# Optimization experiments

Hardware: AMD Instinct MI355X
Metric: run time of the kernel (lower is better)

Reference implementation:

```python
import jax, jax.numpy as jnp
import numpy as np

N_STEPS = 4  # fixed-step RK4 stand-in for dopri5 (jit-friendly, same ODE math)

def mlp(params, tt, z):
    # tt: [N,1] time, z: [N,dim] -> velocity [N,dim]
    W1, b1, W2, b2, W3, b3 = params
    h = jnp.tanh(jnp.concatenate([z, tt], axis=-1) @ W1 + b1)
    h = jnp.tanh(h @ W2 + b2)
    return h @ W3 + b3

def f_and_div(params, tt, z):
    # brute-force divergence via dim JVPs (dim=3, exact trace)
    f = lambda zz: mlp(params, tt, zz)
    out = f(z)
    div = jnp.zeros((z.shape[0],), z.dtype)
    for i in range(z.shape[1]):
        tang = jnp.zeros_like(z).at[:, i].set(1.0)
        _, jv = jax.jvp(f, (z,), (tang,))
        div = div + jv[:, i]
    return out, div[:, None]

def dyn(params, s, t0, z):
    # reparametrize per-sample integration t: t0 -> 0 onto s in [0,1]; dt/ds = -t0
    tt = t0 * (1.0 - s)
    f, div = f_and_div(params, tt, z)
    dz = -t0 * f                                   # dz/ds
    ddiv = t0 * div                                # accumulates int_0^{t0} div f dt
    dpen = t0 * jnp.sum(f * f, axis=-1, keepdims=True)  # kinetic-energy OT penalty
    return dz, ddiv, dpen

def integrate_to_t0(params, x, t0):
    h = 1.0 / N_STEPS
    z = x
    d = jnp.zeros((x.shape[0], 1), x.dtype)
    p = jnp.zeros_like(d)
    for k in range(N_STEPS):
        s = k * h
        g = lambda s_, z_: dyn(params, s_, t0, z_)
        k1z, k1d, k1p = g(s, z)
        k2z, k2d, k2p = g(s + 0.5 * h, z + 0.5 * h * k1z)
        k3z, k3d, k3p = g(s + 0.5 * h, z + 0.5 * h * k2z)
        k4z, k4d, k4p = g(s + h, z + h * k3z)
        z = z + (h / 6.0) * (k1z + 2 * k2z + 2 * k3z + k4z)
        d = d + (h / 6.0) * (k1d + 2 * k2d + 2 * k3d + k4d)
        p = p + (h / 6.0) * (k1p + 2 * k2p + 2 * k3p + k4p)
    return z, d, p

def grid_sample_3d_zeros(vol, coords):
    # vol: [D,H,W]; coords: [N,3] in (x,y,z) normalized [-1,1], align_corners=False,
    # padding_mode='zeros' (matches torch grid_sample semantics)
    D, H, W = vol.shape
    px = ((coords[:, 0] + 1.0) * W - 1.0) / 2.0
    py = ((coords[:, 1] + 1.0) * H - 1.0) / 2.0
    pz = ((coords[:, 2] + 1.0) * D - 1.0) / 2.0
    x0 = jnp.floor(px).astype(jnp.int32); y0 = jnp.floor(py).astype(jnp.int32); z0 = jnp.floor(pz).astype(jnp.int32)
    wx1 = px - x0; wy1 = py - y0; wz1 = pz - z0
    out = jnp.zeros(coords.shape[0], vol.dtype)
    for dz_ in (0, 1):
        for dy_ in (0, 1):
            for dx_ in (0, 1):
                ix = x0 + dx_; iy = y0 + dy_; iz = z0 + dz_
                w = (jnp.where(dx_, wx1, 1 - wx1) * jnp.where(dy_, wy1, 1 - wy1)
                     * jnp.where(dz_, wz1, 1 - wz1))
                valid = (ix >= 0) & (ix < W) & (iy >= 0) & (iy < H) & (iz >= 0) & (iz < D)
                v = vol[jnp.clip(iz, 0, D - 1), jnp.clip(iy, 0, H - 1), jnp.clip(ix, 0, W - 1)]
                out = out + jnp.where(valid, v * w, 0.0)
    return out

def setup_inputs() -> dict:
    key = jax.random.key(0)
    ks = jax.random.split(key, 6)
    N, dim, hid, G = 131072, 3, 64, 100
    x = jax.random.normal(ks[0], (N, dim), jnp.float32)
    t = jax.random.uniform(ks[1], (N, 1), jnp.float32)  # in [0,1], some ~0
    W1 = jax.random.normal(ks[2], (dim + 1, hid), jnp.float32) * 0.5
    W2 = jax.random.normal(ks[3], (hid, hid), jnp.float32) * (1.0 / np.sqrt(hid))
    W3 = jax.random.normal(ks[4], (hid, dim), jnp.float32) * (1.0 / np.sqrt(hid))
    base_grid = jax.random.normal(ks[5], (G, G, G, 1), jnp.float32) * 1e-6
    return {"x": x, "t": t, "W1": W1, "b1": jnp.zeros((hid,), jnp.float32),
            "W2": W2, "b2": jnp.zeros((hid,), jnp.float32),
            "W3": W3, "b3": jnp.zeros((dim,), jnp.float32), "base_grid": base_grid}

def reference(x, t, W1, b1, W2, b2, W3, b3, base_grid):
    params = (W1, b1, W2, b2, W3, b3)
    z_end, d_end, _pen = integrate_to_t0(params, x, t)
    mask = (t > 0)  # [N,1]
    z_t0 = jnp.where(mask, z_end, x)
    div_acc = jnp.where(mask, d_end, 0.0)
    vol = base_grid[..., 0]  # [D,H,W] after torch permute(3,0,1,2)
    logp = grid_sample_3d_zeros(vol, z_t0 / 5.0) - div_acc[:, 0]
    return logp
```

## Files before the change

kernel.cpp:

```cpp
#include <hip/hip_runtime.h>
#include <math.h>

#define NSAMP 131072

typedef _Float16 half8v __attribute__((ext_vector_type(8)));
typedef __fp16   fp16x2 __attribute__((ext_vector_type(2)));
typedef __fp16   fp16x4 __attribute__((ext_vector_type(4)));
typedef __fp16   fp16x8 __attribute__((ext_vector_type(8)));
typedef float    f32x4  __attribute__((ext_vector_type(4)));
typedef float    f32x8  __attribute__((ext_vector_type(8)));

__device__ __forceinline__ float fast_tanh(float x) {
    float e = __builtin_amdgcn_exp2f(x * 2.885390081777927f);
    return fmaf(-2.0f, __builtin_amdgcn_rcpf(e + 1.0f), 1.0f);
}

__device__ __forceinline__ half8v pack8rtz(f32x8 v) {
    fp16x2 p0 = __builtin_amdgcn_cvt_pkrtz(v[0], v[1]);
    fp16x2 p1 = __builtin_amdgcn_cvt_pkrtz(v[2], v[3]);
    fp16x2 p2 = __builtin_amdgcn_cvt_pkrtz(v[4], v[5]);
    fp16x2 p3 = __builtin_amdgcn_cvt_pkrtz(v[6], v[7]);
    fp16x4 q0 = __builtin_shufflevector(p0, p1, 0, 1, 2, 3);
    fp16x4 q1 = __builtin_shufflevector(p2, p3, 0, 1, 2, 3);
    fp16x8 r  = __builtin_shufflevector(q0, q1, 0, 1, 2, 3, 4, 5, 6, 7);
    return __builtin_bit_cast(half8v, r);
}

__global__ __launch_bounds__(256, 2)
void cnf_logp_kernel(const float* __restrict__ xin, const float* __restrict__ tin,
                     const float* __restrict__ W1, const float* __restrict__ b1,
                     const float* __restrict__ W2, const float* __restrict__ b2,
                     const float* __restrict__ W3, const float* __restrict__ b3,
                     const float* __restrict__ vol, float* __restrict__ out)
{
    const int tid  = threadIdx.x;
    const int lane = tid & 63;
    const int col  = lane & 15;
    const int g    = lane >> 4;


    half8v A1[4];
    #pragma unroll
    for (int kq = 0; kq < 4; ++kq) {
        half8v a;
        #pragma unroll
        for (int e = 0; e < 8; ++e) a[e] = (_Float16)0.0f;
        const int krow = kq*16 + col;
        #pragma unroll
        for (int e = 0; e < 4; ++e) {
            const float w = W1[e*64 + krow];
            const _Float16 whi = (_Float16)w;
            const _Float16 wlo = (_Float16)(w - (float)whi);
            _Float16 v = (_Float16)0.0f;
            if (g == 0 || g == 2)      v = whi;
            else if (g == 1)           v = wlo;
            else {
                const float bv = b1[krow];
                const _Float16 bhi = (_Float16)bv;
                if (e == 0)      v = bhi;
                else if (e == 1) v = (_Float16)(bv - (float)bhi);
            }
            a[e] = v;
        }
        A1[kq] = a;
    }

    half8v AW2[8];
    half8v AHW[8];
    #pragma unroll
    for (int nt = 0; nt < 4; ++nt) {
        const int j = nt*16 + col;
        const float w3j0 = W3[j*3+0], w3j1 = W3[j*3+1], w3j2 = W3[j*3+2];
        #pragma unroll
        for (int kh = 0; kh < 2; ++kh) {
            #pragma unroll
            for (int e = 0; e < 8; ++e) {
                const int k = kh*32 + 4*g + (e & 3) + 16*(e >> 2);
                const float w2v = W2[k*64 + j];
                const float gv  = W1[0*64+k]*w3j0 + W1[1*64+k]*w3j1 + W1[2*64+k]*w3j2;
                AW2[nt*2 + kh][e] = (_Float16)w2v;
                AHW[nt*2 + kh][e] = (_Float16)(w2v * gv);
            }
        }
    }
    f32x4 b2v[4];
    #pragma unroll
    for (int nt = 0; nt < 4; ++nt) {
        #pragma unroll
        for (int r = 0; r < 4; ++r) b2v[nt][r] = b2[nt*16 + 4*g + r];
    }
    half8v A3[2];
    #pragma unroll
    for (int kp = 0; kp < 2; ++kp) {
        #pragma unroll
        for (int e = 0; e < 8; ++e) {
            const int j = kp*32 + 4*g + (e & 3) + 16*(e >> 2);
            A3[kp][e] = (col < 3) ? (_Float16)W3[j*3 + col] : (_Float16)0.0f;
        }
    }
    const float b3c0 = b3[0], b3c1 = b3[1], b3c2 = b3[2];

    const int idx = blockIdx.x*64 + (tid >> 6)*16 + col;
    const float x0v = xin[idx*3 + 0], x1v = xin[idx*3 + 1], x2v = xin[idx*3 + 2];
    const float t0  = tin[idx];

    float z0 = x0v, z1 = x1v, z2 = x2v;
    float dacc = 0.0f;
    const float hstep = 0.25f;
    float kz0 = 0.f, kz1 = 0.f, kz2 = 0.f;
    float sa0 = 0.f, sa1 = 0.f, sa2 = 0.f;

    const bool g2f = (g == 2), g3f = (g == 3);

    #pragma unroll 1
    for (int it = 0; it < 16; ++it) {
        const int st   = it & 3;
        const int step = it >> 2;
        const float alpha = (st == 0) ? 0.0f : ((st == 3) ? hstep : 0.5f * hstep);
        const float wgt   = (st == 1 || st == 2) ? (hstep * (1.0f/3.0f)) : (hstep * (1.0f/6.0f));
        const float s     = (float)step * hstep + alpha;
        const float zi0 = fmaf(alpha, kz0, z0);
        const float zi1 = fmaf(alpha, kz1, z1);
        const float zi2 = fmaf(alpha, kz2, z2);
        const float tt  = t0 * (1.0f - s);

        const _Float16 z0h = (_Float16)zi0, z1h = (_Float16)zi1,
                       z2h = (_Float16)zi2, tth = (_Float16)tt;
        const _Float16 z0l = (_Float16)(zi0 - (float)z0h);
        const _Float16 z1l = (_Float16)(zi1 - (float)z1h);
        const _Float16 z2l = (_Float16)(zi2 - (float)z2h);
        const _Float16 ttl = (_Float16)(tt  - (float)tth);
        half8v B1;
        #pragma unroll
        for (int e = 0; e < 8; ++e) B1[e] = (_Float16)0.0f;
        B1[0] = g3f ? (_Float16)1.0f : (g2f ? z0l : z0h);
        B1[1] = g3f ? (_Float16)1.0f : (g2f ? z1l : z1h);
        B1[2] = g3f ? (_Float16)0.0f : (g2f ? z2l : z2h);
        B1[3] = g3f ? (_Float16)0.0f : (g2f ? ttl : tth);

        f32x8 hv[2];
        #pragma unroll
        for (int kq = 0; kq < 4; ++kq) {
            f32x4 z4; z4[0]=0.f; z4[1]=0.f; z4[2]=0.f; z4[3]=0.f;
            z4 = __builtin_amdgcn_mfma_f32_16x16x32_f16(A1[kq], B1, z4, 0, 0, 0);
            #pragma unroll
            for (int r = 0; r < 4; ++r)
                hv[kq >> 1][(kq & 1)*4 + r] = fast_tanh(z4[r]);
        }

        half8v BH[2], BQ[2];
        half8v hone;
        #pragma unroll
        for (int e = 0; e < 8; ++e) hone[e] = (_Float16)1.0f;
        #pragma unroll
        for (int kh = 0; kh < 2; ++kh) {
            BH[kh] = pack8rtz(hv[kh]);
            BQ[kh] = hone - BH[kh]*BH[kh];
        }

        f32x4 a2[4], d2[4];
        #pragma unroll
        for (int nt = 0; nt < 4; ++nt) {
            f32x4 acc = b2v[nt];
            acc = __builtin_amdgcn_mfma_f32_16x16x32_f16(AW2[nt*2+0], BH[0], acc, 0, 0, 0);
            acc = __builtin_amdgcn_mfma_f32_16x16x32_f16(AW2[nt*2+1], BH[1], acc, 0, 0, 0);
            a2[nt] = acc;
            f32x4 z4; z4[0]=0.f; z4[1]=0.f; z4[2]=0.f; z4[3]=0.f;
            z4  = __builtin_amdgcn_mfma_f32_16x16x32_f16(AHW[nt*2+0], BQ[0], z4, 0, 0, 0);
            z4  = __builtin_amdgcn_mfma_f32_16x16x32_f16(AHW[nt*2+1], BQ[1], z4, 0, 0, 0);
            d2[nt] = z4;
        }

        f32x8 h2v[2];
        float pdv = 0.0f;
        #pragma unroll
        for (int nt = 0; nt < 4; ++nt) {
            #pragma unroll
            for (int r = 0; r < 4; ++r) {
                const float h2 = fast_tanh(a2[nt][r]);
                h2v[nt >> 1][(nt & 1)*4 + r] = h2;
                const float s2 = fmaf(-h2, h2, 1.0f);
                pdv = fmaf(s2, d2[nt][r], pdv);
            }
        }
        half8v B2h0 = pack8rtz(h2v[0]);
        half8v B2h1 = pack8rtz(h2v[1]);
        f32x4 fD; fD[0]=0.f; fD[1]=0.f; fD[2]=0.f; fD[3]=0.f;
        fD = __builtin_amdgcn_mfma_f32_16x16x32_f16(A3[0], B2h0, fD, 0, 0, 0);
        fD = __builtin_amdgcn_mfma_f32_16x16x32_f16(A3[1], B2h1, fD, 0, 0, 0);

        pdv += __shfl_xor(pdv, 16);
        pdv += __shfl_xor(pdv, 32);
        const float f0 = __shfl(fD[0], col) + b3c0;
        const float f1 = __shfl(fD[1], col) + b3c1;
        const float f2 = __shfl(fD[2], col) + b3c2;

        const float v0 = -t0 * f0, v1 = -t0 * f1, v2 = -t0 * f2;
        const float vd =  t0 * pdv;
        kz0 = v0; kz1 = v1; kz2 = v2;
        dacc = fmaf(wgt, vd, dacc);
        if (st == 0) { sa0 = wgt*v0; sa1 = wgt*v1; sa2 = wgt*v2; }
        else         { sa0 = fmaf(wgt, v0, sa0); sa1 = fmaf(wgt, v1, sa1); sa2 = fmaf(wgt, v2, sa2); }
        if (st == 3) { z0 += sa0; z1 += sa1; z2 += sa2; }
    }

    if (g == 0) {
        const bool m = (t0 > 0.0f);
        const float q0 = m ? z0 : x0v;
        const float q1 = m ? z1 : x1v;
        const float q2 = m ? z2 : x2v;
        const float dfin = m ? dacc : 0.0f;

        const float px = ((q0 * 0.2f + 1.0f) * 100.0f - 1.0f) * 0.5f;
        const float py = ((q1 * 0.2f + 1.0f) * 100.0f - 1.0f) * 0.5f;
        const float pz = ((q2 * 0.2f + 1.0f) * 100.0f - 1.0f) * 0.5f;
        const float fx = floorf(px), fy = floorf(py), fz = floorf(pz);
        const int ix0 = (int)fx, iy0 = (int)fy, iz0 = (int)fz;
        const float wx1 = px - fx, wy1 = py - fy, wz1 = pz - fz;

        float gs = 0.0f;
        #pragma unroll
        for (int c = 0; c < 8; ++c) {
            const int dxc = c & 1, dyc = (c >> 1) & 1, dzc = (c >> 2) & 1;
            const int ix = ix0 + dxc, iy = iy0 + dyc, iz = iz0 + dzc;
            const float w = (dxc ? wx1 : 1.0f - wx1)
                          * (dyc ? wy1 : 1.0f - wy1)
                          * (dzc ? wz1 : 1.0f - wz1);
            if (ix >= 0 && ix < 100 && iy >= 0 && iy < 100 && iz >= 0 && iz < 100)
                gs += vol[(iz * 100 + iy) * 100 + ix] * w;
        }
        out[idx] = gs - dfin;
    }
}

extern "C" void kernel_launch(void* const* d_in, const int* in_sizes, int n_in,
                              void* d_out, int out_size, void* d_ws, size_t ws_size,
                              hipStream_t stream) {
    const float* x    = (const float*)d_in[0];
    const float* t    = (const float*)d_in[1];
    const float* W1   = (const float*)d_in[2];
    const float* b1   = (const float*)d_in[3];
    const float* W2   = (const float*)d_in[4];
    const float* b2   = (const float*)d_in[5];
    const float* W3   = (const float*)d_in[6];
    const float* b3   = (const float*)d_in[7];
    const float* vol  = (const float*)d_in[8];
    float* out = (float*)d_out;

    dim3 grid(NSAMP / 64), block(256);
    cnf_logp_kernel<<<grid, block, 0, stream>>>(x, t, W1, b1, W2, b2, W3, b3, vol, out);
}
```

Measured before the change: 108.3 us.

## Switch MLP matmuls to 32x32x16 MFMA with 32 samples per wavefront

Replaces the 16x16x32 MFMA tiling with 32x32x16 MFMA tiles, so each wavefront handles 32 samples instead of 16 and the grid is halved. The layer-1 split-precision packing is reorganised into two lane halves (hi/lo) with the bias folded into extra K slots. This cuts the MFMA waste from padded K dimensions and the duplicated per-lane work, so fewer lanes sit idle. In exchange, each lane carries 16-element accumulators, which raises register pressure and may lower occupancy.

```diff
diff --git a/kernel.cpp b/kernel.cpp
--- a/kernel.cpp
+++ b/kernel.cpp
@@ -7,24 +7,31 @@
 typedef __fp16   fp16x2 __attribute__((ext_vector_type(2)));
 typedef __fp16   fp16x4 __attribute__((ext_vector_type(4)));
 typedef __fp16   fp16x8 __attribute__((ext_vector_type(8)));
-typedef float    f32x4  __attribute__((ext_vector_type(4)));
-typedef float    f32x8  __attribute__((ext_vector_type(8)));
+typedef float    f32x16 __attribute__((ext_vector_type(16)));
 
 __device__ __forceinline__ float fast_tanh(float x) {
     float e = __builtin_amdgcn_exp2f(x * 2.885390081777927f);
     return fmaf(-2.0f, __builtin_amdgcn_rcpf(e + 1.0f), 1.0f);
 }
 
-__device__ __forceinline__ half8v pack8rtz(f32x8 v) {
-    fp16x2 p0 = __builtin_amdgcn_cvt_pkrtz(v[0], v[1]);
-    fp16x2 p1 = __builtin_amdgcn_cvt_pkrtz(v[2], v[3]);
-    fp16x2 p2 = __builtin_amdgcn_cvt_pkrtz(v[4], v[5]);
-    fp16x2 p3 = __builtin_amdgcn_cvt_pkrtz(v[6], v[7]);
+__device__ __forceinline__ half8v pack8f(float v0, float v1, float v2, float v3,
+                                         float v4, float v5, float v6, float v7) {
+    fp16x2 p0 = __builtin_amdgcn_cvt_pkrtz(v0, v1);
+    fp16x2 p1 = __builtin_amdgcn_cvt_pkrtz(v2, v3);
+    fp16x2 p2 = __builtin_amdgcn_cvt_pkrtz(v4, v5);
+    fp16x2 p3 = __builtin_amdgcn_cvt_pkrtz(v6, v7);
     fp16x4 q0 = __builtin_shufflevector(p0, p1, 0, 1, 2, 3);
     fp16x4 q1 = __builtin_shufflevector(p2, p3, 0, 1, 2, 3);
     fp16x8 r  = __builtin_shufflevector(q0, q1, 0, 1, 2, 3, 4, 5, 6, 7);
     return __builtin_bit_cast(half8v, r);
 }
+__device__ __forceinline__ half8v pack8lo(const f32x16 v) {
+    return pack8f(v[0], v[1], v[2], v[3], v[4], v[5], v[6], v[7]);
+}
+__device__ __forceinline__ half8v pack8hi(const f32x16 v) {
+    return pack8f(v[8], v[9], v[10], v[11], v[12], v[13], v[14], v[15]);
+}
+
 
 __global__ __launch_bounds__(256, 2)
 void cnf_logp_kernel(const float* __restrict__ xin, const float* __restrict__ tin,
@@ -35,72 +42,77 @@
 {
     const int tid  = threadIdx.x;
     const int lane = tid & 63;
-    const int col  = lane & 15;
-    const int g    = lane >> 4;
-
-
-    half8v A1[4];
-    #pragma unroll
-    for (int kq = 0; kq < 4; ++kq) {
+    const int col  = lane & 31;
+    const int g2   = lane >> 5;
+
+    half8v A1[2];
+    #pragma unroll
+    for (int rt = 0; rt < 2; ++rt) {
         half8v a;
-        #pragma unroll
-        for (int e = 0; e < 8; ++e) a[e] = (_Float16)0.0f;
-        const int krow = kq*16 + col;
+        const int krow = rt*32 + col;
         #pragma unroll
         for (int e = 0; e < 4; ++e) {
             const float w = W1[e*64 + krow];
             const _Float16 whi = (_Float16)w;
             const _Float16 wlo = (_Float16)(w - (float)whi);
-            _Float16 v = (_Float16)0.0f;
-            if (g == 0 || g == 2)      v = whi;
-            else if (g == 1)           v = wlo;
-            else {
-                const float bv = b1[krow];
-                const _Float16 bhi = (_Float16)bv;
-                if (e == 0)      v = bhi;
-                else if (e == 1) v = (_Float16)(bv - (float)bhi);
-            }
-            a[e] = v;
-        }
-        A1[kq] = a;
+            a[e] = g2 ? wlo : whi;
+        }
+        const float bv = b1[krow];
+        const _Float16 bhi = (_Float16)bv;
+        const _Float16 blo = (_Float16)(bv - (float)bhi);
+        a[4] = g2 ? (_Float16)0.0f : bhi;
+        a[5] = g2 ? (_Float16)0.0f : blo;
+        a[6] = (_Float16)0.0f;
+        a[7] = (_Float16)0.0f;
+        A1[rt] = a;
     }
 
     half8v AW2[8];
     half8v AHW[8];
     #pragma unroll
-    for (int nt = 0; nt < 4; ++nt) {
-        const int j = nt*16 + col;
+    for (int jt = 0; jt < 2; ++jt) {
+        const int j = jt*32 + col;
         const float w3j0 = W3[j*3+0], w3j1 = W3[j*3+1], w3j2 = W3[j*3+2];
         #pragma unroll
-        for (int kh = 0; kh < 2; ++kh) {
+        for (int kt = 0; kt < 4; ++kt) {
+            half8v w2q, hq;
             #pragma unroll
             for (int e = 0; e < 8; ++e) {
-                const int k = kh*32 + 4*g + (e & 3) + 16*(e >> 2);
+                const int k = kt*16 + 4*g2 + (e & 3) + 8*(e >> 2);
                 const float w2v = W2[k*64 + j];
                 const float gv  = W1[0*64+k]*w3j0 + W1[1*64+k]*w3j1 + W1[2*64+k]*w3j2;
-                AW2[nt*2 + kh][e] = (_Float16)w2v;
-                AHW[nt*2 + kh][e] = (_Float16)(w2v * gv);
+                w2q[e] = (_Float16)w2v;
+                hq[e]  = (_Float16)(w2v * gv);
             }
-        }
-    }
-    f32x4 b2v[4];
-    #pragma unroll
-    for (int nt = 0; nt < 4; ++nt) {
-        #pragma unroll
-        for (int r = 0; r < 4; ++r) b2v[nt][r] = b2[nt*16 + 4*g + r];
-    }
-    half8v A3[2];
-    #pragma unroll
-    for (int kp = 0; kp < 2; ++kp) {
+            AW2[jt*4 + kt] = w2q;
+            AHW[jt*4 + kt] = hq;
+        }
+    }
+    f32x16 b2C0, b2C1;
+    #pragma unroll
+    for (int reg = 0; reg < 16; ++reg) {
+        const int jr = (reg & 3) + 8*(reg >> 2) + 4*g2;
+        b2C0[reg] = b2[jr];
+        b2C1[reg] = b2[32 + jr];
+    }
+    half8v A3[4];
+    #pragma unroll
+    for (int kt = 0; kt < 4; ++kt) {
+        half8v a;
         #pragma unroll
         for (int e = 0; e < 8; ++e) {
-            const int j = kp*32 + 4*g + (e & 3) + 16*(e >> 2);
-            A3[kp][e] = (col < 3) ? (_Float16)W3[j*3 + col] : (_Float16)0.0f;
-        }
+            const int j = kt*16 + 4*g2 + (e & 3) + 8*(e >> 2);
+            a[e] = (col < 3) ? (_Float16)W3[j*3 + col] : (_Float16)0.0f;
+        }
+        A3[kt] = a;
     }
     const float b3c0 = b3[0], b3c1 = b3[1], b3c2 = b3[2];
 
-    const int idx = blockIdx.x*64 + (tid >> 6)*16 + col;
+    f32x16 zc;
+    #pragma unroll
+    for (int i = 0; i < 16; ++i) zc[i] = 0.0f;
+
+    const int idx = blockIdx.x*128 + (tid >> 6)*32 + col;
     const float x0v = xin[idx*3 + 0], x1v = xin[idx*3 + 1], x2v = xin[idx*3 + 2];
     const float t0  = tin[idx];
 
@@ -109,8 +121,6 @@
     const float hstep = 0.25f;
     float kz0 = 0.f, kz1 = 0.f, kz2 = 0.f;
     float sa0 = 0.f, sa1 = 0.f, sa2 = 0.f;
-
-    const bool g2f = (g == 2), g3f = (g == 3);
 
     #pragma unroll 1
     for (int it = 0; it < 16; ++it) {
@@ -130,70 +140,67 @@
         const _Float16 z1l = (_Float16)(zi1 - (float)z1h);
         const _Float16 z2l = (_Float16)(zi2 - (float)z2h);
         const _Float16 ttl = (_Float16)(tt  - (float)tth);
-        half8v B1;
-        #pragma unroll
-        for (int e = 0; e < 8; ++e) B1[e] = (_Float16)0.0f;
-        B1[0] = g3f ? (_Float16)1.0f : (g2f ? z0l : z0h);
-        B1[1] = g3f ? (_Float16)1.0f : (g2f ? z1l : z1h);
-        B1[2] = g3f ? (_Float16)0.0f : (g2f ? z2l : z2h);
-        B1[3] = g3f ? (_Float16)0.0f : (g2f ? ttl : tth);
-
-        f32x8 hv[2];
-        #pragma unroll
-        for (int kq = 0; kq < 4; ++kq) {
-            f32x4 z4; z4[0]=0.f; z4[1]=0.f; z4[2]=0.f; z4[3]=0.f;
-            z4 = __builtin_amdgcn_mfma_f32_16x16x32_f16(A1[kq], B1, z4, 0, 0, 0);
+        half8v B1v;
+        B1v[0] = g2 ? z0l : z0h;
+        B1v[1] = g2 ? z1l : z1h;
+        B1v[2] = g2 ? z2l : z2h;
+        B1v[3] = g2 ? ttl : tth;
+        B1v[4] = g2 ? (_Float16)0.0f : (_Float16)1.0f;
+        B1v[5] = g2 ? (_Float16)0.0f : (_Float16)1.0f;
+        B1v[6] = (_Float16)0.0f;
+        B1v[7] = (_Float16)0.0f;
+
+        f32x16 hC0 = __builtin_amdgcn_mfma_f32_32x32x16_f16(A1[0], B1v, zc, 0, 0, 0);
+        f32x16 hC1 = __builtin_amdgcn_mfma_f32_32x32x16_f16(A1[1], B1v, zc, 0, 0, 0);
+        f32x16 hv0, hv1;
+        #pragma unroll
+        for (int r = 0; r < 16; ++r) { hv0[r] = fast_tanh(hC0[r]); }
+        #pragma unroll
+        for (int r = 0; r < 16; ++r) { hv1[r] = fast_tanh(hC1[r]); }
+
+        half8v BH[4], BQ[4];
+        BH[0] = pack8lo(hv0); BH[1] = pack8hi(hv0);
+        BH[2] = pack8lo(hv1); BH[3] = pack8hi(hv1);
+        half8v hone;
+        #pragma unroll
+        for (int e = 0; e < 8; ++e) hone[e] = (_Float16)1.0f;
+        #pragma unroll
+        for (int kt = 0; kt < 4; ++kt) BQ[kt] = hone - BH[kt]*BH[kt];
+
+        half8v B2h[4];
+        float pdv = 0.0f;
+        #pragma unroll
+        for (int jt = 0; jt < 2; ++jt) {
+            f32x16 a2C = jt ? b2C1 : b2C0;
+            a2C = __builtin_amdgcn_mfma_f32_32x32x16_f16(AW2[jt*4+0], BH[0], a2C, 0, 0, 0);
+            a2C = __builtin_amdgcn_mfma_f32_32x32x16_f16(AW2[jt*4+1], BH[1], a2C, 0, 0, 0);
+            a2C = __builtin_amdgcn_mfma_f32_32x32x16_f16(AW2[jt*4+2], BH[2], a2C, 0, 0, 0);
+            a2C = __builtin_amdgcn_mfma_f32_32x32x16_f16(AW2[jt*4+3], BH[3], a2C, 0, 0, 0);
+            f32x16 d2C = __builtin_amdgcn_mfma_f32_32x32x16_f16(AHW[jt*4+0], BQ[0], zc, 0, 0, 0);
+            d2C = __builtin_amdgcn_mfma_f32_32x32x16_f16(AHW[jt*4+1], BQ[1], d2C, 0, 0, 0);
+            d2C = __builtin_amdgcn_mfma_f32_32x32x16_f16(AHW[jt*4+2], BQ[2], d2C, 0, 0, 0);
+            d2C = __builtin_amdgcn_mfma_f32_32x32x16_f16(AHW[jt*4+3], BQ[3], d2C, 0, 0, 0);
+            f32x16 h2v_;
             #pragma unroll
-            for (int r = 0; r < 4; ++r)
-                hv[kq >> 1][(kq & 1)*4 + r] = fast_tanh(z4[r]);
-        }
-
-        half8v BH[2], BQ[2];
-        half8v hone;
-        #pragma unroll
-        for (int e = 0; e < 8; ++e) hone[e] = (_Float16)1.0f;
-        #pragma unroll
-        for (int kh = 0; kh < 2; ++kh) {
-            BH[kh] = pack8rtz(hv[kh]);
-            BQ[kh] = hone - BH[kh]*BH[kh];
-        }
-
-        f32x4 a2[4], d2[4];
-        #pragma unroll
-        for (int nt = 0; nt < 4; ++nt) {
-            f32x4 acc = b2v[nt];
-            acc = __builtin_amdgcn_mfma_f32_16x16x32_f16(AW2[nt*2+0], BH[0], acc, 0, 0, 0);
-            acc = __builtin_amdgcn_mfma_f32_16x16x32_f16(AW2[nt*2+1], BH[1], acc, 0, 0, 0);
-            a2[nt] = acc;
-            f32x4 z4; z4[0]=0.f; z4[1]=0.f; z4[2]=0.f; z4[3]=0.f;
-            z4  = __builtin_amdgcn_mfma_f32_16x16x32_f16(AHW[nt*2+0], BQ[0], z4, 0, 0, 0);
-            z4  = __builtin_amdgcn_mfma_f32_16x16x32_f16(AHW[nt*2+1], BQ[1], z4, 0, 0, 0);
-            d2[nt] = z4;
-        }
-
-        f32x8 h2v[2];
-        float pdv = 0.0f;
-        #pragma unroll
-        for (int nt = 0; nt < 4; ++nt) {
-            #pragma unroll
-            for (int r = 0; r < 4; ++r) {
-                const float h2 = fast_tanh(a2[nt][r]);
-                h2v[nt >> 1][(nt & 1)*4 + r] = h2;
+            for (int r = 0; r < 16; ++r) {
+                const float h2 = fast_tanh(a2C[r]);
+                h2v_[r] = h2;
                 const float s2 = fmaf(-h2, h2, 1.0f);
-                pdv = fmaf(s2, d2[nt][r], pdv);
+                pdv = fmaf(s2, d2C[r], pdv);
             }
-        }
-        half8v B2h0 = pack8rtz(h2v[0]);
-        half8v B2h1 = pack8rtz(h2v[1]);
-        f32x4 fD; fD[0]=0.f; fD[1]=0.f; fD[2]=0.f; fD[3]=0.f;
-        fD = __builtin_amdgcn_mfma_f32_16x16x32_f16(A3[0], B2h0, fD, 0, 0, 0);
-        fD = __builtin_amdgcn_mfma_f32_16x16x32_f16(A3[1], B2h1, fD, 0, 0, 0);
-
-        pdv += __shfl_xor(pdv, 16);
+            B2h[jt*2 + 0] = pack8lo(h2v_);
+            B2h[jt*2 + 1] = pack8hi(h2v_);
+        }
+
+        f32x16 fDC = __builtin_amdgcn_mfma_f32_32x32x16_f16(A3[0], B2h[0], zc, 0, 0, 0);
+        fDC = __builtin_amdgcn_mfma_f32_32x32x16_f16(A3[1], B2h[1], fDC, 0, 0, 0);
+        fDC = __builtin_amdgcn_mfma_f32_32x32x16_f16(A3[2], B2h[2], fDC, 0, 0, 0);
+        fDC = __builtin_amdgcn_mfma_f32_32x32x16_f16(A3[3], B2h[3], fDC, 0, 0, 0);
+
         pdv += __shfl_xor(pdv, 32);
-        const float f0 = __shfl(fD[0], col) + b3c0;
-        const float f1 = __shfl(fD[1], col) + b3c1;
-        const float f2 = __shfl(fD[2], col) + b3c2;
+        const float f0 = __shfl(fDC[0], col) + b3c0;
+        const float f1 = __shfl(fDC[1], col) + b3c1;
+        const float f2 = __shfl(fDC[2], col) + b3c2;
 
         const float v0 = -t0 * f0, v1 = -t0 * f1, v2 = -t0 * f2;
         const float vd =  t0 * pdv;
@@ -204,7 +211,7 @@
         if (st == 3) { z0 += sa0; z1 += sa1; z2 += sa2; }
     }
 
-    if (g == 0) {
+    if (g2 == 0) {
         const bool m = (t0 > 0.0f);
         const float q0 = m ? z0 : x0v;
         const float q1 = m ? z1 : x1v;
@@ -247,6 +254,6 @@
     const float* vol  = (const float*)d_in[8];
     float* out = (float*)d_out;
 
-    dim3 grid(NSAMP / 64), block(256);
+    dim3 grid(NSAMP / 128), block(256);
     cnf_logp_kernel<<<grid, block, 0, stream>>>(x, t, W1, b1, W2, b2, W3, b3, vol, out);
 }
```

New measurement: 90.49 us. 16.4% less time.
